# Performance work log

Hardware: AMD Instinct MI355X
Metric: run time of the kernel (lower is better)

Reference implementation:

```python
import jax, jax.numpy as jnp
import numpy as np

N_NODES = 50000
N_EDGES = 800000
D_IN = 128
D_HID = 128
N_CLS = 47


def setup_inputs() -> dict:
    key = jax.random.key(0)
    ks = jax.random.split(key, 10)
    inp = {
        "features": jax.random.normal(ks[0], (N_NODES, D_IN), dtype=jnp.float32),
        "src": jax.random.randint(ks[1], (N_EDGES,), 0, N_NODES),
        "dst": jax.random.randint(ks[2], (N_EDGES,), 0, N_NODES),
        "Wself0": jax.random.normal(ks[3], (D_IN, D_HID), dtype=jnp.float32) / np.sqrt(D_IN),
        "Wneigh0": jax.random.normal(ks[4], (D_IN, D_HID), dtype=jnp.float32) / np.sqrt(D_IN),
        "b0": jnp.zeros((D_HID,), dtype=jnp.float32),
        "Wself1": jax.random.normal(ks[5], (D_HID, D_HID), dtype=jnp.float32) / np.sqrt(D_HID),
        "Wneigh1": jax.random.normal(ks[6], (D_HID, D_HID), dtype=jnp.float32) / np.sqrt(D_HID),
        "b1": jnp.zeros((D_HID,), dtype=jnp.float32),
        "Wself2": jax.random.normal(ks[7], (D_HID, N_CLS), dtype=jnp.float32) / np.sqrt(D_HID),
        "Wneigh2": jax.random.normal(ks[8], (D_HID, N_CLS), dtype=jnp.float32) / np.sqrt(D_HID),
        "b2": jnp.zeros((N_CLS,), dtype=jnp.float32),
    }
    return inp


def reference(features, src, dst, Wself0, Wneigh0, b0, Wself1, Wneigh1, b1, Wself2, Wneigh2, b2):
    # GraphSAGE (DGL SAGEConv, aggregator_type='mean', eval mode so dropout is identity).
    # Per layer: h_neigh[v] = mean_{(u->v) in E} h[u]; out = h @ W_self + h_neigh @ W_neigh + b
    n = features.shape[0]
    # in-degree for mean aggregation (zero-degree nodes get zero neighbor feature)
    deg = jax.ops.segment_sum(jnp.ones(dst.shape, dtype=features.dtype), dst, num_segments=n)
    inv_deg = (1.0 / jnp.maximum(deg, 1.0))[:, None]  # [N,1]

    def sage_layer(h, Ws, Wn, b, act):
        # gather src features per edge, scatter-add into dst, normalize by in-degree
        agg = jax.ops.segment_sum(h[src], dst, num_segments=n) * inv_deg  # [N, d]
        out = h @ Ws + agg @ Wn + b
        return jax.nn.relu(out) if act else out

    h = sage_layer(features, Wself0, Wneigh0, b0, True)
    h = sage_layer(h, Wself1, Wneigh1, b1, True)
    h = sage_layer(h, Wself2, Wneigh2, b2, False)
    return h
```

## Files before the change

kernel.cpp:

```cpp
#include <hip/hip_runtime.h>

#define D 128
#define NCLS 47

typedef short short8 __attribute__((ext_vector_type(8)));
typedef float floatx4 __attribute__((ext_vector_type(4)));

__device__ __forceinline__ float bf16lo(unsigned int u) {
    union { unsigned int i; float f; } c; c.i = u << 16; return c.f;
}
__device__ __forceinline__ float bf16hi(unsigned int u) {
    union { unsigned int i; float f; } c; c.i = u & 0xffff0000u; return c.f;
}
__device__ __forceinline__ unsigned short f2bf(float f) {
    union { float f; unsigned int i; } c; c.f = f;
    unsigned int r = c.i + 0x7fffu + ((c.i >> 16) & 1u);
    return (unsigned short)(r >> 16);
}
__device__ __forceinline__ unsigned int pack2(float x, float y) {
    return (unsigned int)f2bf(x) | ((unsigned int)f2bf(y) << 16);
}

#define FBm 1024
__global__ __launch_bounds__(256) void fill_prep_kernel(
    const int* __restrict__ src, const int* __restrict__ dst,
    int* __restrict__ cnt0, int* __restrict__ cnt1,
    unsigned short* __restrict__ csr, int n_edges,
    const float* __restrict__ f, unsigned int* __restrict__ hA,
    unsigned int* __restrict__ hBz, int npairs, int n,
    const float* __restrict__ Ws0, const float* __restrict__ Wn0, unsigned short* __restrict__ Wt0,
    const float* __restrict__ Ws1, const float* __restrict__ Wn1, unsigned short* __restrict__ Wt1,
    const float* __restrict__ Ws2, const float* __restrict__ Wn2, unsigned short* __restrict__ Wt2) {
    if (blockIdx.x < FBm) {
        int cohort = blockIdx.x & 7;
        int cb = blockIdx.x >> 3;
        int nth = (FBm >> 3) * 256;
        int tid = cb * 256 + threadIdx.x;
        int range = (n + 7) >> 3;
        int lo = cohort * range;
        int hi = lo + range;
        if (hi > n) hi = n;
        const int4* dst4 = (const int4*)dst;
        int nq = n_edges >> 2;
        for (int q = tid; q < nq; q += nth) {
            int4 dd = dst4[q];
            int e = q << 2;
            if (dd.x >= lo && dd.x < hi) {
                int p = atomicAdd(&cnt0[dd.x], 1);
                if (p < 32) csr[dd.x * 64 + p] = (unsigned short)src[e];
            }
            if (dd.y >= lo && dd.y < hi) {
                int p = atomicAdd(&cnt1[dd.y], 1);
                if (p < 32) csr[dd.y * 64 + 32 + p] = (unsigned short)src[e + 1];
            }
            if (dd.z >= lo && dd.z < hi) {
                int p = atomicAdd(&cnt0[dd.z], 1);
                if (p < 32) csr[dd.z * 64 + p] = (unsigned short)src[e + 2];
            }
            if (dd.w >= lo && dd.w < hi) {
                int p = atomicAdd(&cnt1[dd.w], 1);
                if (p < 32) csr[dd.w * 64 + 32 + p] = (unsigned short)src[e + 3];
            }
        }
        for (int e = (nq << 2) + tid; e < n_edges; e += nth) {
            int d = dst[e];
            if (d >= lo && d < hi) {
                if (e & 1) {
                    int p = atomicAdd(&cnt1[d], 1);
                    if (p < 32) csr[d * 64 + 32 + p] = (unsigned short)src[e];
                } else {
                    int p = atomicAdd(&cnt0[d], 1);
                    if (p < 32) csr[d * 64 + p] = (unsigned short)src[e];
                }
            }
        }
        return;
    }
    int tid = (blockIdx.x - FBm) * 256 + threadIdx.x;
    int stride = (gridDim.x - FBm) * 256;
    int total = npairs + 2 * 128 * 256 + 64 * 256 + 64;
    for (int gid = tid; gid < total; gid += stride) {
        if (gid < npairs) {
            if (gid < npairs - 64) {
                float2 v = ((const float2*)f)[gid];
                hA[gid] = pack2(v.x, v.y);
            } else {
                hA[gid] = 0u;
            }
            continue;
        }
        int r = gid - npairs;
        if (r < 128 * 256) {
            int nn = r >> 8, k = r & 255;
            float v = (k < 128) ? Ws0[k * 128 + nn] : Wn0[(k - 128) * 128 + nn];
            Wt0[nn * 256 + k] = f2bf(v);
            continue;
        }
        r -= 128 * 256;
        if (r < 128 * 256) {
            int nn = r >> 8, k = r & 255;
            float v = (k < 128) ? Ws1[k * 128 + nn] : Wn1[(k - 128) * 128 + nn];
            Wt1[nn * 256 + k] = f2bf(v);
            continue;
        }
        r -= 128 * 256;
        if (r < 64 * 256) {
            int nn = r >> 8, k = r & 255;
            float v = 0.0f;
            if (nn < NCLS) v = (k < 128) ? Ws2[k * NCLS + nn] : Wn2[(k - 128) * NCLS + nn];
            Wt2[nn * 256 + k] = f2bf(v);
            continue;
        }
        r -= 64 * 256;
        if (r < 64) hBz[(size_t)n * 64 + r] = 0u;
    }
}

__global__ __launch_bounds__(256, 6) void sage_fused_kernel(
    const unsigned int* __restrict__ hself,
    const unsigned int* __restrict__ hagg,
    const unsigned short* __restrict__ csr,
    const int* __restrict__ cnt0,
    const int* __restrict__ cnt1,
    const unsigned short* __restrict__ Wt,
    const float* __restrict__ bias,
    unsigned short* __restrict__ hout,
    float* __restrict__ out,
    int n, int mode) {
    __shared__ unsigned int selfl[16][68];
    __shared__ unsigned int aggl[16][68];
    __shared__ __align__(16) unsigned short idxl[16][64];
    __shared__ int dl[16];

    int wave = threadIdx.x >> 6;
    int lane = threadIdx.x & 63;
    int base = blockIdx.x * 16;
    const uint4* hs4 = (const uint4*)hself;

    {
        int rowi = threadIdx.x >> 4;
        int q = threadIdx.x & 15;
        int ns = base + rowi;
        unsigned sent = (unsigned)n;
        uint4 sv; sv.x = 0u; sv.y = 0u; sv.z = 0u; sv.w = 0u;
        int c0 = 0, c1 = 0;
        if (ns < n) {
            sv = hs4[(size_t)ns * 16 + q];
            c0 = cnt0[ns]; if (c0 > 32) c0 = 32;
            c1 = cnt1[ns]; if (c1 > 32) c1 = 32;
        }
        *(uint4*)&selfl[rowi][q * 4] = sv;
        int d = c0 + c1;
        const unsigned short* crow = csr + (size_t)ns * 64;
        int j = q * 4;
        unsigned e0 = (j     < d) ? (unsigned)crow[j     < c0 ? j     : 32 + j     - c0] : sent;
        unsigned e1 = (j + 1 < d) ? (unsigned)crow[j + 1 < c0 ? j + 1 : 32 + j + 1 - c0] : sent;
        unsigned e2 = (j + 2 < d) ? (unsigned)crow[j + 2 < c0 ? j + 2 : 32 + j + 2 - c0] : sent;
        unsigned e3 = (j + 3 < d) ? (unsigned)crow[j + 3 < c0 ? j + 3 : 32 + j + 3 - c0] : sent;
        unsigned int* ip = (unsigned int*)&idxl[rowi][0];
        ip[q * 2]     = e0 | (e1 << 16);
        ip[q * 2 + 1] = e2 | (e3 << 16);
        if (q == 0) dl[rowi] = d;
    }
    __syncthreads();

    int sg = lane >> 4;
    int fl = lane & 15;
    int li = wave * 4 + sg;
    int d = dl[li];
    int dp = (d + 7) & ~7;
    const unsigned short* myidx = &idxl[li][0];
    float inv = 1.0f / fmaxf((float)d, 1.0f);

    if (mode == 1) {
#pragma unroll
        for (int p = 0; p < 4; ++p) {
            const unsigned int* bp = hagg + p * 16 + fl;
            float ax = 0.f, ay = 0.f;
            for (int k = 0; k < dp; k += 8) {
                uint4 iq = *(const uint4*)(myidx + k);
                unsigned i0 = iq.x & 0xffffu, i1 = iq.x >> 16;
                unsigned i2 = iq.y & 0xffffu, i3 = iq.y >> 16;
                unsigned i4 = iq.z & 0xffffu, i5 = iq.z >> 16;
                unsigned i6 = iq.w & 0xffffu, i7 = iq.w >> 16;
                unsigned u0 = bp[(size_t)i0 * 64];
                unsigned u1 = bp[(size_t)i1 * 64];
                unsigned u2 = bp[(size_t)i2 * 64];
                unsigned u3 = bp[(size_t)i3 * 64];
                unsigned u4 = bp[(size_t)i4 * 64];
                unsigned u5 = bp[(size_t)i5 * 64];
                unsigned u6 = bp[(size_t)i6 * 64];
                unsigned u7 = bp[(size_t)i7 * 64];
                ax += bf16lo(u0); ay += bf16hi(u0);
                ax += bf16lo(u1); ay += bf16hi(u1);
                ax += bf16lo(u2); ay += bf16hi(u2);
                ax += bf16lo(u3); ay += bf16hi(u3);
                ax += bf16lo(u4); ay += bf16hi(u4);
                ax += bf16lo(u5); ay += bf16hi(u5);
                ax += bf16lo(u6); ay += bf16hi(u6);
                ax += bf16lo(u7); ay += bf16hi(u7);
            }
            aggl[li][p * 16 + fl] = pack2(ax * inv, ay * inv);
        }
    } else {
#pragma unroll
        for (int p = 0; p < 2; ++p) {
            const unsigned int* bp = hagg + p * 16 + fl;
            float ax = 0.f, ay = 0.f;
            for (int k = 0; k < dp; k += 8) {
                uint4 iq = *(const uint4*)(myidx + k);
                unsigned i0 = iq.x & 0xffffu, i1 = iq.x >> 16;
                unsigned i2 = iq.y & 0xffffu, i3 = iq.y >> 16;
                unsigned i4 = iq.z & 0xffffu, i5 = iq.z >> 16;
                unsigned i6 = iq.w & 0xffffu, i7 = iq.w >> 16;
                unsigned u0 = bp[(size_t)i0 * 32];
                unsigned u1 = bp[(size_t)i1 * 32];
                unsigned u2 = bp[(size_t)i2 * 32];
                unsigned u3 = bp[(size_t)i3 * 32];
                unsigned u4 = bp[(size_t)i4 * 32];
                unsigned u5 = bp[(size_t)i5 * 32];
                unsigned u6 = bp[(size_t)i6 * 32];
                unsigned u7 = bp[(size_t)i7 * 32];
                ax += bf16lo(u0); ay += bf16hi(u0);
                ax += bf16lo(u1); ay += bf16hi(u1);
                ax += bf16lo(u2); ay += bf16hi(u2);
                ax += bf16lo(u3); ay += bf16hi(u3);
                ax += bf16lo(u4); ay += bf16hi(u4);
                ax += bf16lo(u5); ay += bf16hi(u5);
                ax += bf16lo(u6); ay += bf16hi(u6);
                ax += bf16lo(u7); ay += bf16hi(u7);
            }
            int j = p * 16 + fl;
            float* fr = (float*)&aggl[li][0];
            fr[2 * j] = ax * inv;
            fr[2 * j + 1] = ay * inv;
        }
    }
    __syncthreads();

    int m = lane & 15;
    int quad = lane >> 4;
    const unsigned short* arow = (const unsigned short*)&selfl[m][0];

    if (mode == 1) {
        const unsigned short* lrow = (const unsigned short*)&aggl[m][0];
        int t0 = wave * 2;
        floatx4 acc[2];
        acc[0] = (floatx4){0.f, 0.f, 0.f, 0.f};
        acc[1] = (floatx4){0.f, 0.f, 0.f, 0.f};
#pragma unroll
        for (int ko = 0; ko < 128; ko += 32) {
            short8 av = *(const short8*)(arow + ko + quad * 8);
#pragma unroll
            for (int tt = 0; tt < 2; ++tt) {
                short8 bfr = *(const short8*)(Wt + (size_t)((t0 + tt) * 16 + m) * 256 + ko + quad * 8);
                acc[tt] = __builtin_amdgcn_mfma_f32_16x16x32_bf16(av, bfr, acc[tt], 0, 0, 0);
            }
        }
#pragma unroll
        for (int ko = 0; ko < 128; ko += 32) {
            short8 av = *(const short8*)(lrow + ko + quad * 8);
#pragma unroll
            for (int tt = 0; tt < 2; ++tt) {
                short8 bfr = *(const short8*)(Wt + (size_t)((t0 + tt) * 16 + m) * 256 + 128 + ko + quad * 8);
                acc[tt] = __builtin_amdgcn_mfma_f32_16x16x32_bf16(av, bfr, acc[tt], 0, 0, 0);
            }
        }
#pragma unroll
        for (int tt = 0; tt < 2; ++tt) {
            int nfeat = (t0 + tt) * 16 + m;
            float bb = bias[nfeat];
#pragma unroll
            for (int r = 0; r < 4; ++r) {
                int node = base + quad * 4 + r;
                if (node < n) {
                    float v = fmaxf(acc[tt][r] + bb, 0.0f);
                    hout[(size_t)node * 128 + nfeat] = f2bf(v);
                }
            }
        }
    } else {
        int t0 = wave;
        if (wave < 3) {
            floatx4 acc = (floatx4){0.f, 0.f, 0.f, 0.f};
#pragma unroll
            for (int ko = 0; ko < 128; ko += 32) {
                short8 av = *(const short8*)(arow + ko + quad * 8);
                short8 bfr = *(const short8*)(Wt + (size_t)(t0 * 16 + m) * 256 + ko + quad * 8);
                acc = __builtin_amdgcn_mfma_f32_16x16x32_bf16(av, bfr, acc, 0, 0, 0);
            }
            int nfeat = t0 * 16 + m;
            if (nfeat < NCLS) {
                float bb = bias[nfeat];
#pragma unroll
                for (int r = 0; r < 4; ++r) {
                    int node = base + quad * 4 + r;
                    if (node < n) {
                        const float* fr = (const float*)&aggl[quad * 4 + r][0];
                        out[(size_t)node * NCLS + nfeat] = acc[r] + fr[nfeat] + bb;
                    }
                }
            }
        }
    }
}

__global__ __launch_bounds__(256) void proj_kernel(
    const unsigned int* __restrict__ hin,
    const unsigned short* __restrict__ Wt,
    unsigned short* __restrict__ P,
    int np) {
    __shared__ unsigned int sl[16][68];
    int wave = threadIdx.x >> 6;
    int lane = threadIdx.x & 63;
    int pb = blockIdx.x * 16;
    const uint4* h4 = (const uint4*)hin;
    {
        int rowi = threadIdx.x >> 4;
        int q = threadIdx.x & 15;
        int ns = pb + rowi;
        uint4 sv; sv.x = 0u; sv.y = 0u; sv.z = 0u; sv.w = 0u;
        if (ns < np) sv = h4[(size_t)ns * 16 + q];
        *(uint4*)&sl[rowi][q * 4] = sv;
    }
    __syncthreads();
    int m = lane & 15;
    int quad = lane >> 4;
    const unsigned short* arow = (const unsigned short*)&sl[m][0];
    floatx4 acc = (floatx4){0.f, 0.f, 0.f, 0.f};
#pragma unroll
    for (int ko = 0; ko < 128; ko += 32) {
        short8 av = *(const short8*)(arow + ko + quad * 8);
        short8 bfr = *(const short8*)(Wt + (size_t)(wave * 16 + m) * 256 + 128 + ko + quad * 8);
        acc = __builtin_amdgcn_mfma_f32_16x16x32_bf16(av, bfr, acc, 0, 0, 0);
    }
    int col = wave * 16 + m;
#pragma unroll
    for (int r = 0; r < 4; ++r) {
        int node = pb + quad * 4 + r;
        if (node < np) P[(size_t)node * 64 + col] = f2bf(acc[r]);
    }
}

extern "C" void kernel_launch(void* const* d_in, const int* in_sizes, int n_in,
                              void* d_out, int out_size, void* d_ws, size_t ws_size,
                              hipStream_t stream) {
    const float* features = (const float*)d_in[0];
    const int* src = (const int*)d_in[1];
    const int* dst = (const int*)d_in[2];
    const float* Ws0 = (const float*)d_in[3];
    const float* Wn0 = (const float*)d_in[4];
    const float* b0 = (const float*)d_in[5];
    const float* Ws1 = (const float*)d_in[6];
    const float* Wn1 = (const float*)d_in[7];
    const float* b1 = (const float*)d_in[8];
    const float* Ws2 = (const float*)d_in[9];
    const float* Wn2 = (const float*)d_in[10];
    const float* b2 = (const float*)d_in[11];
    float* out = (float*)d_out;

    int n = in_sizes[0] / D;
    int n_edges = in_sizes[1];
    int np1 = n + 1;

    int* cnt0 = (int*)d_ws;
    int* cnt1 = cnt0 + 50048;
    unsigned short* csr = (unsigned short*)(cnt1 + 50048);
    unsigned int* hA = (unsigned int*)(csr + (size_t)n * 64 + 32);
    unsigned int* hB = hA + (size_t)np1 * 64;
    unsigned short* Wt0 = (unsigned short*)(hB + (size_t)np1 * 64);
    unsigned short* Wt1 = Wt0 + 128 * 256;
    unsigned short* Wt2 = Wt1 + 128 * 256;
    unsigned short* P = (unsigned short*)(Wt2 + 64 * 256);

    int npairs = np1 * 64;

    hipMemsetAsync(cnt0, 0, (size_t)2 * 50048 * sizeof(int), stream);
    fill_prep_kernel<<<2048, 256, 0, stream>>>(
        src, dst, cnt0, cnt1, csr, n_edges, features, hA, hB, npairs, n,
        Ws0, Wn0, Wt0, Ws1, Wn1, Wt1, Ws2, Wn2, Wt2);

    int tiles = (n + 15) / 16;

    sage_fused_kernel<<<tiles, 256, 0, stream>>>(hA, hA, csr, cnt0, cnt1, Wt0, b0,
                                                 (unsigned short*)hB, nullptr, n, 1);
    sage_fused_kernel<<<tiles, 256, 0, stream>>>(hB, hB, csr, cnt0, cnt1, Wt1, b1,
                                                 (unsigned short*)hA, nullptr, n, 1);
    proj_kernel<<<(np1 + 15) / 16, 256, 0, stream>>>(hA, Wt2, P, np1);
    sage_fused_kernel<<<tiles, 256, 0, stream>>>(hA, (const unsigned int*)P, csr, cnt0, cnt1,
                                                 Wt2, b2, nullptr, out, n, 2);
}
```

Before: 280.5 us.

## Stage neighbor gathers through LDS with async global_load_lds double buffering

The neighbor aggregation now has each wave process its four nodes one at a time. Each neighbor row is fetched as 16-byte chunks with global_load_lds directly into a per-wave double-buffered LDS staging area, then reduced from LDS. Before, each lane issued scattered 4-byte global loads per neighbor. The launch-bounds occupancy hint rises from 6 to 8 blocks per SM. This trades wider coalesced loads and async prefetch against serialized per-node loops, extra LDS traffic, per-step waitcnt stalls and added LDS use per block.

```diff
diff --git a/kernel.cpp b/kernel.cpp
--- a/kernel.cpp
+++ b/kernel.cpp
@@ -5,6 +5,9 @@
 
 typedef short short8 __attribute__((ext_vector_type(8)));
 typedef float floatx4 __attribute__((ext_vector_type(4)));
+
+typedef __attribute__((address_space(3))) unsigned int lds_uint;
+typedef const __attribute__((address_space(1))) unsigned int glb_uint;
 
 __device__ __forceinline__ float bf16lo(unsigned int u) {
     union { unsigned int i; float f; } c; c.i = u << 16; return c.f;
@@ -20,6 +23,12 @@
 __device__ __forceinline__ unsigned int pack2(float x, float y) {
     return (unsigned int)f2bf(x) | ((unsigned int)f2bf(y) << 16);
 }
+
+__device__ __forceinline__ void gload_lds16(const unsigned int* g, unsigned int* l) {
+    __builtin_amdgcn_global_load_lds((glb_uint*)g, (lds_uint*)l, 16, 0, 0);
+}
+#define WAITVM0 asm volatile("s_waitcnt vmcnt(0)" ::: "memory")
+#define WAITVM1 asm volatile("s_waitcnt vmcnt(1)" ::: "memory")
 
 #define FBm 1024
 __global__ __launch_bounds__(256) void fill_prep_kernel(
@@ -116,7 +125,7 @@
     }
 }
 
-__global__ __launch_bounds__(256, 6) void sage_fused_kernel(
+__global__ __launch_bounds__(256, 8) void sage_fused_kernel(
     const unsigned int* __restrict__ hself,
     const unsigned int* __restrict__ hagg,
     const unsigned short* __restrict__ csr,
@@ -131,6 +140,7 @@
     __shared__ unsigned int aggl[16][68];
     __shared__ __align__(16) unsigned short idxl[16][64];
     __shared__ int dl[16];
+    __shared__ unsigned int sbuf[4][512];
 
     int wave = threadIdx.x >> 6;
     int lane = threadIdx.x & 63;
@@ -164,76 +174,85 @@
     }
     __syncthreads();
 
-    int sg = lane >> 4;
-    int fl = lane & 15;
-    int li = wave * 4 + sg;
-    int d = dl[li];
-    int dp = (d + 7) & ~7;
-    const unsigned short* myidx = &idxl[li][0];
-    float inv = 1.0f / fmaxf((float)d, 1.0f);
+    unsigned int* sbw = &sbuf[wave][0];
 
     if (mode == 1) {
-#pragma unroll
-        for (int p = 0; p < 4; ++p) {
-            const unsigned int* bp = hagg + p * 16 + fl;
+        int l4 = (lane >> 4);
+        int lc = (lane & 15) * 4;
+        for (int i = 0; i < 4; ++i) {
+            int li = wave * 4 + i;
+            int d = dl[li];
+            int nst = (d + 3) >> 2;
             float ax = 0.f, ay = 0.f;
-            for (int k = 0; k < dp; k += 8) {
-                uint4 iq = *(const uint4*)(myidx + k);
-                unsigned i0 = iq.x & 0xffffu, i1 = iq.x >> 16;
-                unsigned i2 = iq.y & 0xffffu, i3 = iq.y >> 16;
-                unsigned i4 = iq.z & 0xffffu, i5 = iq.z >> 16;
-                unsigned i6 = iq.w & 0xffffu, i7 = iq.w >> 16;
-                unsigned u0 = bp[(size_t)i0 * 64];
-                unsigned u1 = bp[(size_t)i1 * 64];
-                unsigned u2 = bp[(size_t)i2 * 64];
-                unsigned u3 = bp[(size_t)i3 * 64];
-                unsigned u4 = bp[(size_t)i4 * 64];
-                unsigned u5 = bp[(size_t)i5 * 64];
-                unsigned u6 = bp[(size_t)i6 * 64];
-                unsigned u7 = bp[(size_t)i7 * 64];
-                ax += bf16lo(u0); ay += bf16hi(u0);
-                ax += bf16lo(u1); ay += bf16hi(u1);
-                ax += bf16lo(u2); ay += bf16hi(u2);
-                ax += bf16lo(u3); ay += bf16hi(u3);
-                ax += bf16lo(u4); ay += bf16hi(u4);
-                ax += bf16lo(u5); ay += bf16hi(u5);
-                ax += bf16lo(u6); ay += bf16hi(u6);
-                ax += bf16lo(u7); ay += bf16hi(u7);
-            }
-            aggl[li][p * 16 + fl] = pack2(ax * inv, ay * inv);
+            if (nst > 0) {
+                {
+                    unsigned ridx = idxl[li][l4];
+                    gload_lds16(hagg + (size_t)ridx * 64 + lc, sbw);
+                }
+                for (int s = 1; s < nst; ++s) {
+                    unsigned ridx = idxl[li][s * 4 + l4];
+                    gload_lds16(hagg + (size_t)ridx * 64 + lc, sbw + (s & 1) * 256);
+                    WAITVM1;
+                    const unsigned int* sp = sbw + ((s - 1) & 1) * 256 + lane;
+#pragma unroll
+                    for (int j = 0; j < 4; ++j) {
+                        unsigned u = sp[j * 64];
+                        ax += bf16lo(u); ay += bf16hi(u);
+                    }
+                }
+                WAITVM0;
+                const unsigned int* sp = sbw + ((nst - 1) & 1) * 256 + lane;
+#pragma unroll
+                for (int j = 0; j < 4; ++j) {
+                    unsigned u = sp[j * 64];
+                    ax += bf16lo(u); ay += bf16hi(u);
+                }
+            }
+            float inv = 1.0f / fmaxf((float)d, 1.0f);
+            aggl[li][lane] = pack2(ax * inv, ay * inv);
         }
     } else {
-#pragma unroll
-        for (int p = 0; p < 2; ++p) {
-            const unsigned int* bp = hagg + p * 16 + fl;
+        int l8 = (lane >> 3);
+        int lc = (lane & 7) * 4;
+        int col = lane & 31;
+        int half = lane >> 5;
+        for (int i = 0; i < 4; ++i) {
+            int li = wave * 4 + i;
+            int d = dl[li];
+            int nst = (d + 7) >> 3;
             float ax = 0.f, ay = 0.f;
-            for (int k = 0; k < dp; k += 8) {
-                uint4 iq = *(const uint4*)(myidx + k);
-                unsigned i0 = iq.x & 0xffffu, i1 = iq.x >> 16;
-                unsigned i2 = iq.y & 0xffffu, i3 = iq.y >> 16;
-                unsigned i4 = iq.z & 0xffffu, i5 = iq.z >> 16;
-                unsigned i6 = iq.w & 0xffffu, i7 = iq.w >> 16;
-                unsigned u0 = bp[(size_t)i0 * 32];
-                unsigned u1 = bp[(size_t)i1 * 32];
-                unsigned u2 = bp[(size_t)i2 * 32];
-                unsigned u3 = bp[(size_t)i3 * 32];
-                unsigned u4 = bp[(size_t)i4 * 32];
-                unsigned u5 = bp[(size_t)i5 * 32];
-                unsigned u6 = bp[(size_t)i6 * 32];
-                unsigned u7 = bp[(size_t)i7 * 32];
-                ax += bf16lo(u0); ay += bf16hi(u0);
-                ax += bf16lo(u1); ay += bf16hi(u1);
-                ax += bf16lo(u2); ay += bf16hi(u2);
-                ax += bf16lo(u3); ay += bf16hi(u3);
-                ax += bf16lo(u4); ay += bf16hi(u4);
-                ax += bf16lo(u5); ay += bf16hi(u5);
-                ax += bf16lo(u6); ay += bf16hi(u6);
-                ax += bf16lo(u7); ay += bf16hi(u7);
-            }
-            int j = p * 16 + fl;
-            float* fr = (float*)&aggl[li][0];
-            fr[2 * j] = ax * inv;
-            fr[2 * j + 1] = ay * inv;
+            if (nst > 0) {
+                {
+                    unsigned ridx = idxl[li][l8];
+                    gload_lds16(hagg + (size_t)ridx * 32 + lc, sbw);
+                }
+                for (int s = 1; s < nst; ++s) {
+                    unsigned ridx = idxl[li][s * 8 + l8];
+                    gload_lds16(hagg + (size_t)ridx * 32 + lc, sbw + (s & 1) * 256);
+                    WAITVM1;
+                    const unsigned int* sp = sbw + ((s - 1) & 1) * 256 + half * 128 + col;
+#pragma unroll
+                    for (int j = 0; j < 4; ++j) {
+                        unsigned u = sp[j * 32];
+                        ax += bf16lo(u); ay += bf16hi(u);
+                    }
+                }
+                WAITVM0;
+                const unsigned int* sp = sbw + ((nst - 1) & 1) * 256 + half * 128 + col;
+#pragma unroll
+                for (int j = 0; j < 4; ++j) {
+                    unsigned u = sp[j * 32];
+                    ax += bf16lo(u); ay += bf16hi(u);
+                }
+            }
+            ax += __shfl_xor(ax, 32, 64);
+            ay += __shfl_xor(ay, 32, 64);
+            if (half == 0) {
+                float inv = 1.0f / fmaxf((float)d, 1.0f);
+                float* fr = (float*)&aggl[li][0];
+                fr[2 * col] = ax * inv;
+                fr[2 * col + 1] = ay * inv;
+            }
         }
     }
     __syncthreads();
@@ -280,16 +299,15 @@
             }
         }
     } else {
-        int t0 = wave;
         if (wave < 3) {
             floatx4 acc = (floatx4){0.f, 0.f, 0.f, 0.f};
 #pragma unroll
             for (int ko = 0; ko < 128; ko += 32) {
                 short8 av = *(const short8*)(arow + ko + quad * 8);
-                short8 bfr = *(const short8*)(Wt + (size_t)(t0 * 16 + m) * 256 + ko + quad * 8);
+                short8 bfr = *(const short8*)(Wt + (size_t)(wave * 16 + m) * 256 + ko + quad * 8);
                 acc = __builtin_amdgcn_mfma_f32_16x16x32_bf16(av, bfr, acc, 0, 0, 0);
             }
-            int nfeat = t0 * 16 + m;
+            int nfeat = wave * 16 + m;
             if (nfeat < NCLS) {
                 float bb = bias[nfeat];
 #pragma unroll
```

After: 282.4 us. Within noise of the previous version (+0.7%).
